# Optimization experiments

Measured on AMD Instinct MI355X. Metric: run time of the kernel, lower is better.

The kernel has to match this reference:

```python
import jax, jax.numpy as jnp
import numpy as np

B, N, D = 1, 4096, 512
H, HD = 8, 64
NBINS = 512
CAND = 64
SCALE = 1.0 / np.sqrt(HD)
MAX_NORM = 1.0 - 1e-5
TWO_PI = 2.0 * np.pi


def _project(x):
    # Poincare-ball style projection: clip L2 norm of each point to MAX_NORM.
    n = jnp.sqrt(jnp.sum(x * x, axis=-1, keepdims=True))
    s = jnp.minimum(1.0, MAX_NORM / jnp.maximum(n, 1e-12))
    return x * s


def _bins(x):
    # Deterministic geometric binning (DavisCache stand-in): quantize the
    # angle of the first two coordinates into NBINS bins.
    ang = jnp.arctan2(x[..., 1], x[..., 0])  # (-pi, pi]
    b = jnp.floor((ang / TWO_PI + 0.5) * NBINS)
    return jnp.clip(b, 0, NBINS - 1).astype(jnp.int32)


def setup_inputs() -> dict:
    key0 = jax.random.key(0)
    ks = jax.random.split(key0, 12)
    w = 0.02  # typical init scale for projection weights
    return {
        "query": jax.random.normal(ks[0], (B, N, D), dtype=jnp.float32),
        "key": jax.random.normal(ks[1], (B, N, D), dtype=jnp.float32),
        "value": jax.random.normal(ks[2], (B, N, D), dtype=jnp.float32),
        "Wq": jax.random.normal(ks[3], (D, D), dtype=jnp.float32) * w,
        "bq": jnp.zeros((D,), dtype=jnp.float32),
        "Wk": jax.random.normal(ks[4], (D, D), dtype=jnp.float32) * w,
        "bk": jnp.zeros((D,), dtype=jnp.float32),
        "Wv": jax.random.normal(ks[5], (D, D), dtype=jnp.float32) * w,
        "bv": jnp.zeros((D,), dtype=jnp.float32),
        "Wo": jax.random.normal(ks[6], (D, D), dtype=jnp.float32) * w,
        "bo": jnp.zeros((D,), dtype=jnp.float32),
    }


def reference(query, key, value, Wq, bq, Wk, bk, Wv, bv, Wo, bo):
    Bq, Nq, Dm = query.shape
    Nk = key.shape[1]
    # projections + split heads -> (B, H, N, HD)
    q = (query @ Wq.T + bq).reshape(Bq, Nq, H, HD).transpose(0, 2, 1, 3)
    k = (key @ Wk.T + bk).reshape(Bq, Nk, H, HD).transpose(0, 2, 1, 3)
    v = (value @ Wv.T + bv).reshape(Bq, Nk, H, HD).transpose(0, 2, 1, 3)
    q = _project(q)
    k = _project(k)

    # geometric binning; candidate keys for a query are those whose bin is
    # within radius 1 of the query's bin (neighboring_bins, radius=1).
    qb = _bins(q)  # (B, H, Nq) int32
    kb = _bins(k)  # (B, H, Nk) int32
    mask = jnp.abs(qb[..., :, None] - kb[..., None, :]) <= 1  # (B,H,Nq,Nk)
    # fallback: if a query has no candidates, attend over all keys
    any_valid = jnp.any(mask, axis=-1, keepdims=True)
    eff = jnp.where(any_valid, mask, True)
    # keep only the first CAND candidates per query (by key index)
    rank = jnp.cumsum(eff.astype(jnp.int32), axis=-1) - 1
    sel = eff & (rank < CAND)

    scores = jnp.einsum("bhqd,bhkd->bhqk", q, k) * SCALE
    scores = jnp.where(sel, scores, -jnp.inf)
    attn = jax.nn.softmax(scores, axis=-1)  # dropout p=0.0 (eval mode)
    out = jnp.einsum("bhqk,bhkd->bhqd", attn, v)

    out = out.transpose(0, 2, 1, 3).reshape(Bq, Nq, Dm)
    return out @ Wo.T + bo
```

## Files before the change

kernel.cpp:

```cpp
#include <hip/hip_runtime.h>
#include <math.h>

typedef unsigned short u16;
typedef __attribute__((ext_vector_type(8))) short v8bf;
typedef __attribute__((ext_vector_type(4))) float f32x4;

#define N_TOK 4096
#define DMODEL 512
#define NHEAD 8
#define HDIM 64
#define CANDN 64
#define NBINS 512
#define BINCAP 64
#define QCAP 128
#define ATT_SCALE 0.125f
#define MAX_NORM_F 0.99999f

__device__ __forceinline__ u16 f2bf(float f) {
  union { float f; unsigned int i; } v; v.f = f;
  unsigned int x = v.i;
  return (u16)((x + 0x7fffu + ((x >> 16) & 1u)) >> 16);
}
__device__ __forceinline__ uint4 pack8v(const float4 x0, const float4 x1) {
  union { u16 h[8]; uint4 u; } r;
  r.h[0] = f2bf(x0.x); r.h[1] = f2bf(x0.y); r.h[2] = f2bf(x0.z); r.h[3] = f2bf(x0.w);
  r.h[4] = f2bf(x1.x); r.h[5] = f2bf(x1.y); r.h[6] = f2bf(x1.z); r.h[7] = f2bf(x1.w);
  return r.u;
}

__device__ float fdlibm_atanf(float x) {
#pragma clang fp contract(off)
  const float atanhi[4] = {4.6364760399e-01f, 7.8539812565e-01f,
                           9.8279368877e-01f, 1.5707962513e+00f};
  const float atanlo[4] = {5.0121582440e-09f, 3.7748947079e-08f,
                           3.4473217170e-08f, 7.5497894159e-08f};
  const float aT[5] = {3.3333328366e-01f, -1.9999158382e-01f, 1.4253635705e-01f,
                       -1.0648017377e-01f, 6.1687607318e-02f};
  unsigned ix = __float_as_uint(x);
  const unsigned sign = ix >> 31;
  ix &= 0x7fffffffu;
  int id;
  float z, w, s1, s2;
  if (ix >= 0x4c800000u) {
    z = atanhi[3] + 0x1p-120f;
    return sign ? -z : z;
  }
  if (ix < 0x3ee00000u) {
    if (ix < 0x39800000u) return x;
    id = -1;
  } else {
    x = fabsf(x);
    if (ix < 0x3f980000u) {
      if (ix < 0x3f300000u) { id = 0; x = (2.0f * x - 1.0f) / (2.0f + x); }
      else                  { id = 1; x = (x - 1.0f) / (x + 1.0f); }
    } else {
      if (ix < 0x401c0000u) { id = 2; x = (x - 1.5f) / (1.0f + 1.5f * x); }
      else                  { id = 3; x = -1.0f / x; }
    }
  }
  z = x * x;
  w = z * z;
  s1 = z * (aT[0] + w * (aT[2] + w * aT[4]));
  s2 = w * (aT[1] + w * aT[3]);
  if (id < 0) return x - x * (s1 + s2);
  z = atanhi[id] - ((x * (s1 + s2) - atanlo[id]) - x);
  return sign ? -z : z;
}

__device__ float fdlibm_atan2f(float y, float x) {
#pragma clang fp contract(off)
  const float pi = 3.1415927410e+00f, pi_lo = -8.7422776573e-08f;
  const unsigned hx = __float_as_uint(x), hy = __float_as_uint(y);
  if (hx == 0x3f800000u) return fdlibm_atanf(y);
  const unsigned m = ((hy >> 31) & 1u) | ((hx >> 30) & 2u);
  const unsigned ix = hx & 0x7fffffffu, iy = hy & 0x7fffffffu;
  if (iy == 0u) {
    switch (m) { case 0: case 1: return y; case 2: return pi; default: return -pi; }
  }
  if (ix == 0u) return (m & 1u) ? -1.57079637050628662f : 1.57079637050628662f;
  float z;
  if (ix + (26u << 23) < iy) {
    z = 1.57079637050628662f;
    return (m & 1u) ? -z : z;
  }
  if ((m & 2u) && iy + (26u << 23) < ix) z = 0.0f;
  else z = fdlibm_atanf(fabsf(y / x));
  switch (m) {
    case 0: return z;
    case 1: return -z;
    case 2: return pi - (z - pi_lo);
    default: return (z - pi_lo) - pi;
  }
}

__global__ __launch_bounds__(256) void binsfix_kernel(
    const float* __restrict__ query, const float* __restrict__ key_,
    const float* __restrict__ Wq, const float* __restrict__ Wk,
    int* __restrict__ qb, int* __restrict__ kb, int* __restrict__ khist)
{
  __shared__ float xs[16 * 516];
  __shared__ float wsh[16 * 516];
  __shared__ int wle[64];
  __shared__ int wlc;
  const int blk = blockIdx.x;
  const int tid = threadIdx.x;

  if (blk >= 512) {
    int4 z4; z4.x = 0; z4.y = 0; z4.z = 0; z4.w = 0;
#pragma unroll
    for (int i = 0; i < 8; ++i) ((int4*)khist)[tid + i * 256] = z4;
    return;
  }

  const int isk  = blk >> 8;
  const int tile = blk & 255;
  const float* X = isk ? key_ : query;
  const float* W = isk ? Wk : Wq;

#pragma unroll
  for (int i = 0; i < 8; ++i) {
    const int flat = i * 1024 + tid * 4;
    const int row = flat >> 9, col = flat & 511;
    *(float4*)&xs[row * 516 + col] = *(const float4*)(X + (tile * 16 + row) * DMODEL + col);
  }
#pragma unroll
  for (int i = 0; i < 8; ++i) {
    const int f = i * 256 + tid;
    const int row = f >> 7;
    const int col = (f & 127) * 4;
    const int wrow = ((row >> 1) << 6) | (row & 1);
    *(float4*)&wsh[row * 516 + col] = *(const float4*)(W + wrow * DMODEL + col);
  }
  if (tid == 0) wlc = 0;
  __syncthreads();

  {
    const int n_local = tid >> 4;
    const int pair = tid & 15;
    const int h = pair >> 1, coord = pair & 1;
    const float* wrow = &wsh[pair * 516];
    const float* xrow = &xs[n_local * 516];

    double c0 = 0.0, c1 = 0.0, c2 = 0.0, c3 = 0.0;
#pragma unroll 4
    for (int k = 0; k < DMODEL; k += 4) {
      const float4 xv = *(const float4*)(xrow + k);
      const float4 wv = *(const float4*)(wrow + k);
      c0 = fma((double)xv.x, (double)wv.x, c0);
      c1 = fma((double)xv.y, (double)wv.y, c1);
      c2 = fma((double)xv.z, (double)wv.z, c2);
      c3 = fma((double)xv.w, (double)wv.w, c3);
    }
    const double a = (c0 + c1) + (c2 + c3);
    const double other = __shfl_xor(a, 1);
    if (coord == 0) {
      const double a0 = a, a1 = other;
      const int n = tile * 16 + n_local;
      double ang = atan2(a1, a0);
      double t = (ang / 6.283185307179586 + 0.5) * 512.0;
      int b = (int)floor(t);
      b = b < 0 ? 0 : (b > 511 ? 511 : b);

      const double r = sqrt(a0 * a0 + a1 * a1);
      const double dist = fabs(t - nearbyint(t));
      const double margin = fmin(0.45, 3.3e-4 / fmax(r, 1e-30) + 5e-5);
      if (dist < margin) {
        const int p = atomicAdd(&wlc, 1);
        if (p < 64) wle[p] = (h << 4) | n_local;
        else (isk ? kb : qb)[(h << 12) + n] = b;
      } else {
        (isk ? kb : qb)[(h << 12) + n] = b;
      }
    }
  }
  __syncthreads();

  int nw = wlc; if (nw > 64) nw = 64;
  const int w = tid >> 6, d = tid & 63;
  for (int e = w; e < nw; e += 4) {
    const int n_local2 = wle[e] & 15;
    const int h2 = wle[e] >> 4;
    const int n = tile * 16 + n_local2;
    const float* xr = &xs[n_local2 * 516];
    const float* wr = W + ((h2 << 6) + d) * DMODEL;
    float acc = 0.0f;
    for (int k = 0; k < DMODEL; k += 16) {
      const float4 xa = *(const float4*)(xr + k);
      const float4 xb = *(const float4*)(xr + k + 4);
      const float4 xc = *(const float4*)(xr + k + 8);
      const float4 xd = *(const float4*)(xr + k + 12);
      const float4 wa = *(const float4*)(wr + k);
      const float4 wb = *(const float4*)(wr + k + 4);
      const float4 wc = *(const float4*)(wr + k + 8);
      const float4 wd = *(const float4*)(wr + k + 12);
      acc = __fmaf_rn(xa.x, wa.x, acc); acc = __fmaf_rn(xa.y, wa.y, acc);
      acc = __fmaf_rn(xa.z, wa.z, acc); acc = __fmaf_rn(xa.w, wa.w, acc);
      acc = __fmaf_rn(xb.x, wb.x, acc); acc = __fmaf_rn(xb.y, wb.y, acc);
      acc = __fmaf_rn(xb.z, wb.z, acc); acc = __fmaf_rn(xb.w, wb.w, acc);
      acc = __fmaf_rn(xc.x, wc.x, acc); acc = __fmaf_rn(xc.y, wc.y, acc);
      acc = __fmaf_rn(xc.z, wc.z, acc); acc = __fmaf_rn(xc.w, wc.w, acc);
      acc = __fmaf_rn(xd.x, wd.x, acc); acc = __fmaf_rn(xd.y, wd.y, acc);
      acc = __fmaf_rn(xd.z, wd.z, acc); acc = __fmaf_rn(xd.w, wd.w, acc);
    }
    {
#pragma clang fp contract(off)
      const float sq = acc * acc;
      float rr[8];
#pragma unroll
      for (int j = 0; j < 8; ++j) rr[j] = __shfl(sq, j);
      for (int i = 8; i < 64; i += 8) {
#pragma unroll
        for (int j = 0; j < 8; ++j) rr[j] += __shfl(sq, i + j);
      }
      const float ss = ((rr[0] + rr[1]) + (rr[2] + rr[3])) +
                       ((rr[4] + rr[5]) + (rr[6] + rr[7]));
      const float nrm = __fsqrt_rn(ss);
      const float s = fminf(1.0f, 0.99999f / fmaxf(nrm, 1e-12f));
      const float c0 = __shfl(acc, 0) * s;
      const float c1 = __shfl(acc, 1) * s;
      const float cr = (float)atan2((double)c1, (double)c0);
      const float fd = fdlibm_atan2f(c1, c0);
      const float tol = fmaxf(fabsf(cr) * 6e-7f, 1e-30f);
      const float ang = (fabsf(fd - cr) <= tol) ? fd : cr;
      const float t = ((ang / 6.2831854820251465f) + 0.5f) * 512.0f;
      int b = (int)floorf(t);
      b = b < 0 ? 0 : (b > 511 ? 511 : b);
      if (d == 0) (isk ? kb : qb)[(h2 << 12) + n] = b;
    }
  }
}

__global__ __launch_bounds__(256) void gemmhist_kernel(
    const float* __restrict__ query, const float* __restrict__ key_,
    const float* __restrict__ value,
    const float* __restrict__ Wq, const float* __restrict__ Wk,
    const float* __restrict__ Wv,
    const float* __restrict__ bq, const float* __restrict__ bk,
    const float* __restrict__ bv,
    const int* __restrict__ qb, const int* __restrict__ kb,
    int* __restrict__ khist, u16* __restrict__ blist,
    int* __restrict__ qhist, u16* __restrict__ qlist,
    u16* __restrict__ Qb, u16* __restrict__ Kb, u16* __restrict__ Vb)
{
  __shared__ __align__(16) char smem[30720];
  const int blk = blockIdx.x;
  const int tid = threadIdx.x;

  if (blk >= 768) {
    const int rel = blk - 768;
    const int h = rel & 7;
    const int type = (rel >> 3) & 1;
    const int chunk = rel >> 4;
    const int* src = type ? qb : kb;
    int* hist = type ? qhist : khist;
    u16* list = type ? qlist : blist;
    const int cap = type ? QCAP : BINCAP;
    const int i = (chunk << 8) + tid;
    const int b = src[(h << 12) + i];
    const int pos = atomicAdd(&hist[(h << 9) + b], 1);
    if (pos < cap) list[((h << 9) + b) * cap + pos] = (u16)i;
    return;
  }

  u16* As = (u16*)smem;
  u16* Ws = (u16*)(smem + 10240);

  const int z = blk >> 8;
  const int rem = blk & 255;
  const int bm = (rem & 63) * 64;
  const int bn = (rem >> 6) * 128;

  const float* X  = (z == 0) ? query : (z == 1) ? key_ : value;
  const float* WF = (z == 0) ? Wq : (z == 1) ? Wk : Wv;
  const float* bias = (z == 0) ? bq : (z == 1) ? bk : bv;
  u16* O          = (z == 0) ? Qb : (z == 1) ? Kb : Vb;

  const int lane = tid & 63;
  const int wave = tid >> 6;
  const int ra  = tid >> 2;
  const int oa  = (tid & 3) * 8;
  const int wm = (wave & 1) * 32;
  const int wn = (wave >> 1) * 64;
  const int l15 = lane & 15;
  const int quad = lane >> 4;

  f32x4 acc[2][4] = {};

  float4 a0f0 = *(const float4*)(X + (bm + ra) * DMODEL + oa);
  float4 a0f1 = *(const float4*)(X + (bm + ra) * DMODEL + oa + 4);
  float4 w0f0 = *(const float4*)(WF + (bn + ra) * DMODEL + oa);
  float4 w0f1 = *(const float4*)(WF + (bn + ra) * DMODEL + oa + 4);
  float4 w1f0 = *(const float4*)(WF + (bn + ra + 64) * DMODEL + oa);
  float4 w1f1 = *(const float4*)(WF + (bn + ra + 64) * DMODEL + oa + 4);

  for (int kt = 0; kt < DMODEL; kt += 32) {
    const int p = (kt >> 5) & 1;
    *(uint4*)&As[p * 2560 + ra * 40 + oa] = pack8v(a0f0, a0f1);
    *(uint4*)&Ws[p * 5120 + ra * 40 + oa] = pack8v(w0f0, w0f1);
    *(uint4*)&Ws[p * 5120 + (ra + 64) * 40 + oa] = pack8v(w1f0, w1f1);
    __syncthreads();
    if (kt + 32 < DMODEL) {
      a0f0 = *(const float4*)(X + (bm + ra) * DMODEL + kt + 32 + oa);
      a0f1 = *(const float4*)(X + (bm + ra) * DMODEL + kt + 32 + oa + 4);
      w0f0 = *(const float4*)(WF + (bn + ra) * DMODEL + kt + 32 + oa);
      w0f1 = *(const float4*)(WF + (bn + ra) * DMODEL + kt + 32 + oa + 4);
      w1f0 = *(const float4*)(WF + (bn + ra + 64) * DMODEL + kt + 32 + oa);
      w1f1 = *(const float4*)(WF + (bn + ra + 64) * DMODEL + kt + 32 + oa + 4);
    }
    v8bf af[2], bfr[4];
#pragma unroll
    for (int i = 0; i < 2; ++i)
      af[i] = *(const v8bf*)&As[p * 2560 + (wm + i * 16 + l15) * 40 + quad * 8];
#pragma unroll
    for (int j = 0; j < 4; ++j)
      bfr[j] = *(const v8bf*)&Ws[p * 5120 + (wn + j * 16 + l15) * 40 + quad * 8];
#pragma unroll
    for (int i = 0; i < 2; ++i)
#pragma unroll
      for (int j = 0; j < 4; ++j)
        acc[i][j] = __builtin_amdgcn_mfma_f32_16x16x32_bf16(af[i], bfr[j], acc[i][j], 0, 0, 0);
  }

  float bval[4];
#pragma unroll
  for (int j = 0; j < 4; ++j) bval[j] = bias[bn + wn + j * 16 + l15];
  const int h = (bn + wn) >> 6;

#pragma unroll
  for (int i = 0; i < 2; ++i) {
#pragma unroll
    for (int r = 0; r < 4; ++r) {
      const int row = bm + wm + i * 16 + quad * 4 + r;
      float v0 = acc[i][0][r] + bval[0];
      float v1 = acc[i][1][r] + bval[1];
      float v2 = acc[i][2][r] + bval[2];
      float v3 = acc[i][3][r] + bval[3];
      if (z != 2) {
        float ss = v0 * v0 + v1 * v1 + v2 * v2 + v3 * v3;
#pragma unroll
        for (int o = 1; o < 16; o <<= 1) ss += __shfl_xor(ss, o);
        const float s = fminf(1.0f, MAX_NORM_F / fmaxf(sqrtf(ss), 1e-12f));
        v0 *= s; v1 *= s; v2 *= s; v3 *= s;
      }
      const int base = (((h << 12) + row) << 6) + l15;
      O[base +  0] = f2bf(v0); O[base + 16] = f2bf(v1);
      O[base + 32] = f2bf(v2); O[base + 48] = f2bf(v3);
    }
  }
}

__global__ __launch_bounds__(64) void attn_bin_kernel(
    const u16* __restrict__ Qb, const u16* __restrict__ Kb,
    const u16* __restrict__ Vb, const int* __restrict__ qhist,
    const u16* __restrict__ qlist, const int* __restrict__ khist,
    const u16* __restrict__ blist, u16* __restrict__ aout)
{
  __shared__ u16 kf[4 * 2 * 4 * 16 * 8];
  __shared__ u16 pf[16 * 72];
  __shared__ u16 s_cand[64];
  __shared__ int s_qg[16];

  const int hb = blockIdx.x;
  const int h = hb >> 9;
  const int b = hb & 511;
  int qcnt = qhist[hb];
  if (qcnt > QCAP) qcnt = QCAP;
  if (qcnt == 0) return;

  const int lane = threadIdx.x;
  const int l15 = lane & 15;
  const int quad = lane >> 4;

  int v0 = 0xFFFF, v1 = 0xFFFF, v2 = 0xFFFF;
  int c0 = 0, c1 = 0, c2 = 0;
  if (b > 0) {
    c0 = khist[(h << 9) + b - 1];
    if (c0 > BINCAP) c0 = BINCAP;
    if (lane < c0) v0 = (int)blist[(((h << 9) + b - 1) << 6) + lane];
  }
  {
    c1 = khist[(h << 9) + b];
    if (c1 > BINCAP) c1 = BINCAP;
    if (lane < c1) v1 = (int)blist[(((h << 9) + b) << 6) + lane];
  }
  if (b < NBINS - 1) {
    c2 = khist[(h << 9) + b + 1];
    if (c2 > BINCAP) c2 = BINCAP;
    if (lane < c2) v2 = (int)blist[(((h << 9) + b + 1) << 6) + lane];
  }

  int r0 = 0, r1 = 0, r2 = 0;
#pragma unroll 8
  for (int j = 0; j < 64; ++j) {
    const int w0 = __shfl(v0, j);
    const int w1 = __shfl(v1, j);
    const int w2 = __shfl(v2, j);
    r0 += (w0 < v0) + (w1 < v0) + (w2 < v0);
    r1 += (w0 < v1) + (w1 < v1) + (w2 < v1);
    r2 += (w0 < v2) + (w1 < v2) + (w2 < v2);
  }
  const int tot = c0 + c1 + c2;
  const int ccnt = tot < CANDN ? tot : CANDN;
  const int ccnt_eff = (tot == 0) ? 64 : ccnt;
  if (tot == 0) {
    s_cand[lane] = (u16)lane;
  } else {
    if (v0 != 0xFFFF && r0 < CANDN) s_cand[r0] = (u16)v0;
    if (v1 != 0xFFFF && r1 < CANDN) s_cand[r1] = (u16)v1;
    if (v2 != 0xFFFF && r2 < CANDN) s_cand[r2] = (u16)v2;
  }
  __syncthreads();
  if (tot > 0 && lane >= ccnt) s_cand[lane] = s_cand[0];
  __syncthreads();

  {
    const int r = lane >> 3, s = lane & 7;
    const int ks = s >> 2, qd = s & 3;
#pragma unroll
    for (int it = 0; it < 8; ++it) {
      const int key = it * 8 + r;
      const int c = s_cand[key];
      const uint4 kv = *(const uint4*)(Kb + ((h << 18) | (c << 6)) + s * 8);
      const int idx = ((((key >> 4) * 2 + ks) * 4 + qd) * 16 + (key & 15)) * 8;
      *(uint4*)&kf[idx] = kv;
    }
  }
  __syncthreads();
  v8bf akf[4][2];
#pragma unroll
  for (int t = 0; t < 4; ++t)
#pragma unroll
    for (int ks = 0; ks < 2; ++ks)
      akf[t][ks] = *(const v8bf*)&kf[(((t * 2 + ks) * 4 + quad) * 16 + l15) * 8];
  __syncthreads();

  {
    const int r = lane >> 3, s = lane & 7;
    const int nt = s >> 1, d0 = (s & 1) * 8;
#pragma unroll
    for (int it = 0; it < 8; ++it) {
      const int key = it * 8 + r;
      const int c = s_cand[key];
      union { u16 hh[8]; uint4 u; } vv;
      vv.u = *(const uint4*)(Vb + ((h << 18) | (c << 6)) + s * 8);
      const int kstep = key >> 5, qd = (key >> 3) & 3, j = key & 7;
#pragma unroll
      for (int m = 0; m < 8; ++m)
        kf[(((nt * 2 + kstep) * 4 + qd) * 16 + d0 + m) * 8 + j] = vv.hh[m];
    }
  }
  __syncthreads();
  v8bf bvf[4][2];
#pragma unroll
  for (int t = 0; t < 4; ++t)
#pragma unroll
    for (int ks = 0; ks < 2; ++ks)
      bvf[t][ks] = *(const v8bf*)&kf[(((t * 2 + ks) * 4 + quad) * 16 + l15) * 8];

  const int nchunk = (qcnt + 15) >> 4;
  for (int ci = 0; ci < nchunk; ++ci) {
    const int base = ci << 4;
    const int qcn = min(16, qcnt - base);
    __syncthreads();
    if (lane < 16) {
      int idx = base + lane;
      if (idx > qcnt - 1) idx = qcnt - 1;
      s_qg[lane] = (int)qlist[(hb << 7) + idx];
    }
    __syncthreads();

    const u16* qrow = Qb + ((h << 18) | (s_qg[l15] << 6));
    v8bf bq[2];
#pragma unroll
    for (int ks = 0; ks < 2; ++ks)
      bq[ks] = *(const v8bf*)(qrow + ks * 32 + quad * 8);

    float sc[16];
    __builtin_amdgcn_s_setprio(1);
#pragma unroll
    for (int t = 0; t < 4; ++t) {
      f32x4 sa = {0.f, 0.f, 0.f, 0.f};
      sa = __builtin_amdgcn_mfma_f32_16x16x32_bf16(akf[t][0], bq[0], sa, 0, 0, 0);
      sa = __builtin_amdgcn_mfma_f32_16x16x32_bf16(akf[t][1], bq[1], sa, 0, 0, 0);
#pragma unroll
      for (int r = 0; r < 4; ++r) {
        const int key = t * 16 + quad * 4 + r;
        sc[t * 4 + r] = (key < ccnt_eff) ? sa[r] * ATT_SCALE : -INFINITY;
      }
    }
    __builtin_amdgcn_s_setprio(0);
    float mx = sc[0];
#pragma unroll
    for (int i = 1; i < 16; ++i) mx = fmaxf(mx, sc[i]);
    mx = fmaxf(mx, __shfl_xor(mx, 16));
    mx = fmaxf(mx, __shfl_xor(mx, 32));
    float sum = 0.0f;
    float pe[16];
#pragma unroll
    for (int i = 0; i < 16; ++i) { pe[i] = __expf(sc[i] - mx); sum += pe[i]; }
    sum += __shfl_xor(sum, 16);
    sum += __shfl_xor(sum, 32);
    const float inv = 1.0f / sum;

    __syncthreads();
#pragma unroll
    for (int t = 0; t < 4; ++t)
#pragma unroll
      for (int r = 0; r < 4; ++r)
        pf[l15 * 72 + t * 16 + quad * 4 + r] = f2bf(pe[t * 4 + r] * inv);
    __syncthreads();

    v8bf ap[2];
#pragma unroll
    for (int ks = 0; ks < 2; ++ks)
      ap[ks] = *(const v8bf*)&pf[l15 * 72 + ks * 32 + quad * 8];

    __builtin_amdgcn_s_setprio(1);
#pragma unroll
    for (int nt = 0; nt < 4; ++nt) {
      f32x4 o = {0.f, 0.f, 0.f, 0.f};
      o = __builtin_amdgcn_mfma_f32_16x16x32_bf16(ap[0], bvf[nt][0], o, 0, 0, 0);
      o = __builtin_amdgcn_mfma_f32_16x16x32_bf16(ap[1], bvf[nt][1], o, 0, 0, 0);
#pragma unroll
      for (int r = 0; r < 4; ++r) {
        const int row = quad * 4 + r;
        if (row < qcn)
          aout[s_qg[row] * DMODEL + (h << 6) + nt * 16 + l15] = f2bf(o[r]);
      }
    }
    __builtin_amdgcn_s_setprio(0);
  }
}

__global__ __launch_bounds__(256) void gemm_out_kernel(
    const u16* __restrict__ A, const float* __restrict__ WF,
    const float* __restrict__ bias, float* __restrict__ O)
{
  __shared__ u16 As[2][64 * 40];
  __shared__ u16 Ws[2][64 * 40];

  const int tid  = threadIdx.x;
  const int lane = tid & 63;
  const int wave = tid >> 6;
  const int ra  = tid >> 2;
  const int oa  = (tid & 3) * 8;

  const int bm = blockIdx.x * 64;
  const int bn = blockIdx.y * 64;
  const int wm = (wave & 1) * 32;
  const int wn = (wave >> 1) * 32;
  const int l15 = lane & 15;
  const int quad = lane >> 4;

  f32x4 acc[2][2] = {};

  uint4 a0 = *(const uint4*)(A + (bm + ra) * DMODEL + oa);
  float4 w0f0 = *(const float4*)(WF + (bn + ra) * DMODEL + oa);
  float4 w0f1 = *(const float4*)(WF + (bn + ra) * DMODEL + oa + 4);

  for (int kt = 0; kt < DMODEL; kt += 32) {
    const int p = (kt >> 5) & 1;
    *(uint4*)&As[p][ra * 40 + oa] = a0;
    *(uint4*)&Ws[p][ra * 40 + oa] = pack8v(w0f0, w0f1);
    __syncthreads();
    if (kt + 32 < DMODEL) {
      a0 = *(const uint4*)(A + (bm + ra) * DMODEL + kt + 32 + oa);
      w0f0 = *(const float4*)(WF + (bn + ra) * DMODEL + kt + 32 + oa);
      w0f1 = *(const float4*)(WF + (bn + ra) * DMODEL + kt + 32 + oa + 4);
    }
    v8bf af[2], bfr[2];
#pragma unroll
    for (int i = 0; i < 2; ++i)
      af[i] = *(const v8bf*)&As[p][(wm + i * 16 + l15) * 40 + quad * 8];
#pragma unroll
    for (int j = 0; j < 2; ++j)
      bfr[j] = *(const v8bf*)&Ws[p][(wn + j * 16 + l15) * 40 + quad * 8];
#pragma unroll
    for (int i = 0; i < 2; ++i)
#pragma unroll
      for (int j = 0; j < 2; ++j)
        acc[i][j] = __builtin_amdgcn_mfma_f32_16x16x32_bf16(af[i], bfr[j], acc[i][j], 0, 0, 0);
  }

#pragma unroll
  for (int j = 0; j < 2; ++j) {
    const int cg = bn + wn + j * 16 + l15;
    const float bval = bias[cg];
#pragma unroll
    for (int i = 0; i < 2; ++i) {
      const int rbase = bm + wm + i * 16 + quad * 4;
#pragma unroll
      for (int r = 0; r < 4; ++r)
        O[(rbase + r) * DMODEL + cg] = acc[i][j][r] + bval;
    }
  }
}

extern "C" void kernel_launch(void* const* d_in, const int* in_sizes, int n_in,
                              void* d_out, int out_size, void* d_ws, size_t ws_size,
                              hipStream_t stream) {
  const float* query = (const float*)d_in[0];
  const float* key_  = (const float*)d_in[1];
  const float* value = (const float*)d_in[2];
  const float* Wq = (const float*)d_in[3];
  const float* bq = (const float*)d_in[4];
  const float* Wk = (const float*)d_in[5];
  const float* bk = (const float*)d_in[6];
  const float* Wv = (const float*)d_in[7];
  const float* bv = (const float*)d_in[8];
  const float* Wo = (const float*)d_in[9];
  const float* bo = (const float*)d_in[10];

  char* ws = (char*)d_ws;
  u16* Qb    = (u16*)(ws + 14680064);
  u16* Kb    = (u16*)(ws + 18874368);
  u16* Vb    = (u16*)(ws + 23068672);
  u16* aout  = (u16*)(ws + 27262976);
  int* qb    = (int*)(ws + 31457280);
  int* kb    = (int*)(ws + 31588352);
  int* khist = (int*)(ws + 31784960);
  int* qhist = (int*)(ws + 31801344);
  u16* blist = (u16*)(ws + 31817728);
  u16* qlist = (u16*)(ws + 32342016);

  binsfix_kernel<<<513, 256, 0, stream>>>(
      query, key_, Wq, Wk, qb, kb, khist);
  gemmhist_kernel<<<1024, 256, 0, stream>>>(
      query, key_, value, Wq, Wk, Wv, bq, bk, bv,
      qb, kb, khist, blist, qhist, qlist, Qb, Kb, Vb);
  attn_bin_kernel<<<4096, 64, 0, stream>>>(
      Qb, Kb, Vb, qhist, qlist, khist, blist, aout);
  gemm_out_kernel<<<dim3(64, 8), 256, 0, stream>>>(aout, Wo, bo, (float*)d_out);
}
```

Measured before the change: 174.4 us.

## Fuse bin computation, histogram build and QKV GEMM into one kernel launch

```diff
diff --git a/kernel.cpp b/kernel.cpp
--- a/kernel.cpp
+++ b/kernel.cpp
@@ -26,6 +26,11 @@
   r.h[0] = f2bf(x0.x); r.h[1] = f2bf(x0.y); r.h[2] = f2bf(x0.z); r.h[3] = f2bf(x0.w);
   r.h[4] = f2bf(x1.x); r.h[5] = f2bf(x1.y); r.h[6] = f2bf(x1.z); r.h[7] = f2bf(x1.w);
   return r.u;
+}
+
+__global__ __launch_bounds__(256) void zero_hist_kernel(int* __restrict__ khist) {
+  int4 z4; z4.x = 0; z4.y = 0; z4.z = 0; z4.w = 0;
+  ((int4*)khist)[(blockIdx.x << 8) + threadIdx.x] = z4;
 }
 
 __device__ float fdlibm_atanf(float x) {
@@ -93,29 +98,125 @@
   }
 }
 
-__global__ __launch_bounds__(256) void binsfix_kernel(
+__global__ __launch_bounds__(256) void fused_kernel(
     const float* __restrict__ query, const float* __restrict__ key_,
+    const float* __restrict__ value,
     const float* __restrict__ Wq, const float* __restrict__ Wk,
-    int* __restrict__ qb, int* __restrict__ kb, int* __restrict__ khist)
+    const float* __restrict__ Wv,
+    const float* __restrict__ bq, const float* __restrict__ bk,
+    const float* __restrict__ bv,
+    int* __restrict__ qb, int* __restrict__ kb,
+    int* __restrict__ khist, u16* __restrict__ blist,
+    int* __restrict__ qhist, u16* __restrict__ qlist,
+    u16* __restrict__ Qb, u16* __restrict__ Kb, u16* __restrict__ Vb)
 {
-  __shared__ float xs[16 * 516];
-  __shared__ float wsh[16 * 516];
+  __shared__ __align__(16) char smem[66304];
   __shared__ int wle[64];
   __shared__ int wlc;
   const int blk = blockIdx.x;
   const int tid = threadIdx.x;
 
   if (blk >= 512) {
-    int4 z4; z4.x = 0; z4.y = 0; z4.z = 0; z4.w = 0;
-#pragma unroll
-    for (int i = 0; i < 8; ++i) ((int4*)khist)[tid + i * 256] = z4;
+    u16* As = (u16*)smem;
+    u16* Ws = (u16*)(smem + 10240);
+
+    const int rel = blk - 512;
+    const int z = rel >> 8;
+    const int rem = rel & 255;
+    const int bm = (rem & 63) * 64;
+    const int bn = (rem >> 6) * 128;
+
+    const float* X  = (z == 0) ? query : (z == 1) ? key_ : value;
+    const float* WF = (z == 0) ? Wq : (z == 1) ? Wk : Wv;
+    const float* bias = (z == 0) ? bq : (z == 1) ? bk : bv;
+    u16* O          = (z == 0) ? Qb : (z == 1) ? Kb : Vb;
+
+    const int lane = tid & 63;
+    const int wave = tid >> 6;
+    const int ra  = tid >> 2;
+    const int oa  = (tid & 3) * 8;
+    const int wm = (wave & 1) * 32;
+    const int wn = (wave >> 1) * 64;
+    const int l15 = lane & 15;
+    const int quad = lane >> 4;
+
+    f32x4 acc[2][4] = {};
+
+    float4 a0f0 = *(const float4*)(X + (bm + ra) * DMODEL + oa);
+    float4 a0f1 = *(const float4*)(X + (bm + ra) * DMODEL + oa + 4);
+    float4 w0f0 = *(const float4*)(WF + (bn + ra) * DMODEL + oa);
+    float4 w0f1 = *(const float4*)(WF + (bn + ra) * DMODEL + oa + 4);
+    float4 w1f0 = *(const float4*)(WF + (bn + ra + 64) * DMODEL + oa);
+    float4 w1f1 = *(const float4*)(WF + (bn + ra + 64) * DMODEL + oa + 4);
+
+    for (int kt = 0; kt < DMODEL; kt += 32) {
+      const int p = (kt >> 5) & 1;
+      *(uint4*)&As[p * 2560 + ra * 40 + oa] = pack8v(a0f0, a0f1);
+      *(uint4*)&Ws[p * 5120 + ra * 40 + oa] = pack8v(w0f0, w0f1);
+      *(uint4*)&Ws[p * 5120 + (ra + 64) * 40 + oa] = pack8v(w1f0, w1f1);
+      __syncthreads();
+      if (kt + 32 < DMODEL) {
+        a0f0 = *(const float4*)(X + (bm + ra) * DMODEL + kt + 32 + oa);
+        a0f1 = *(const float4*)(X + (bm + ra) * DMODEL + kt + 32 + oa + 4);
+        w0f0 = *(const float4*)(WF + (bn + ra) * DMODEL + kt + 32 + oa);
+        w0f1 = *(const float4*)(WF + (bn + ra) * DMODEL + kt + 32 + oa + 4);
+        w1f0 = *(const float4*)(WF + (bn + ra + 64) * DMODEL + kt + 32 + oa);
+        w1f1 = *(const float4*)(WF + (bn + ra + 64) * DMODEL + kt + 32 + oa + 4);
+      }
+      v8bf af[2], bfr[4];
+#pragma unroll
+      for (int i = 0; i < 2; ++i)
+        af[i] = *(const v8bf*)&As[p * 2560 + (wm + i * 16 + l15) * 40 + quad * 8];
+#pragma unroll
+      for (int j = 0; j < 4; ++j)
+        bfr[j] = *(const v8bf*)&Ws[p * 5120 + (wn + j * 16 + l15) * 40 + quad * 8];
+#pragma unroll
+      for (int i = 0; i < 2; ++i)
+#pragma unroll
+        for (int j = 0; j < 4; ++j)
+          acc[i][j] = __builtin_amdgcn_mfma_f32_16x16x32_bf16(af[i], bfr[j], acc[i][j], 0, 0, 0);
+    }
+
+    float bval[4];
+#pragma unroll
+    for (int j = 0; j < 4; ++j) bval[j] = bias[bn + wn + j * 16 + l15];
+    const int h = (bn + wn) >> 6;
+
+#pragma unroll
+    for (int i = 0; i < 2; ++i) {
+#pragma unroll
+      for (int r = 0; r < 4; ++r) {
+        const int row = bm + wm + i * 16 + quad * 4 + r;
+        float v0 = acc[i][0][r] + bval[0];
+        float v1 = acc[i][1][r] + bval[1];
+        float v2 = acc[i][2][r] + bval[2];
+        float v3 = acc[i][3][r] + bval[3];
+        if (z != 2) {
+          float ss = v0 * v0 + v1 * v1 + v2 * v2 + v3 * v3;
+#pragma unroll
+          for (int o = 1; o < 16; o <<= 1) ss += __shfl_xor(ss, o);
+          const float s = fminf(1.0f, MAX_NORM_F / fmaxf(sqrtf(ss), 1e-12f));
+          v0 *= s; v1 *= s; v2 *= s; v3 *= s;
+        }
+        const int base = (((h << 12) + row) << 6) + l15;
+        O[base +  0] = f2bf(v0); O[base + 16] = f2bf(v1);
+        O[base + 32] = f2bf(v2); O[base + 48] = f2bf(v3);
+      }
+    }
     return;
   }
+
+  float* xs  = (float*)smem;
+  float* wsh = (float*)(smem + 33024);
 
   const int isk  = blk >> 8;
   const int tile = blk & 255;
   const float* X = isk ? key_ : query;
   const float* W = isk ? Wk : Wq;
+  int* outb  = isk ? kb : qb;
+  int* hist  = isk ? khist : qhist;
+  u16* list  = isk ? blist : qlist;
+  const int cap = isk ? BINCAP : QCAP;
 
 #pragma unroll
   for (int i = 0; i < 8; ++i) {
@@ -164,12 +265,15 @@
       const double r = sqrt(a0 * a0 + a1 * a1);
       const double dist = fabs(t - nearbyint(t));
       const double margin = fmin(0.45, 3.3e-4 / fmax(r, 1e-30) + 5e-5);
+      bool deferred = false;
       if (dist < margin) {
         const int p = atomicAdd(&wlc, 1);
-        if (p < 64) wle[p] = (h << 4) | n_local;
-        else (isk ? kb : qb)[(h << 12) + n] = b;
-      } else {
-        (isk ? kb : qb)[(h << 12) + n] = b;
+        if (p < 64) { wle[p] = (h << 4) | n_local; deferred = true; }
+      }
+      if (!deferred) {
+        outb[(h << 12) + n] = b;
+        const int pos = atomicAdd(&hist[(h << 9) + b], 1);
+        if (pos < cap) list[((h << 9) + b) * cap + pos] = (u16)n;
       }
     }
   }
@@ -225,126 +329,11 @@
       const float t = ((ang / 6.2831854820251465f) + 0.5f) * 512.0f;
       int b = (int)floorf(t);
       b = b < 0 ? 0 : (b > 511 ? 511 : b);
-      if (d == 0) (isk ? kb : qb)[(h2 << 12) + n] = b;
-    }
-  }
-}
-
-__global__ __launch_bounds__(256) void gemmhist_kernel(
-    const float* __restrict__ query, const float* __restrict__ key_,
-    const float* __restrict__ value,
-    const float* __restrict__ Wq, const float* __restrict__ Wk,
-    const float* __restrict__ Wv,
-    const float* __restrict__ bq, const float* __restrict__ bk,
-    const float* __restrict__ bv,
-    const int* __restrict__ qb, const int* __restrict__ kb,
-    int* __restrict__ khist, u16* __restrict__ blist,
-    int* __restrict__ qhist, u16* __restrict__ qlist,
-    u16* __restrict__ Qb, u16* __restrict__ Kb, u16* __restrict__ Vb)
-{
-  __shared__ __align__(16) char smem[30720];
-  const int blk = blockIdx.x;
-  const int tid = threadIdx.x;
-
-  if (blk >= 768) {
-    const int rel = blk - 768;
-    const int h = rel & 7;
-    const int type = (rel >> 3) & 1;
-    const int chunk = rel >> 4;
-    const int* src = type ? qb : kb;
-    int* hist = type ? qhist : khist;
-    u16* list = type ? qlist : blist;
-    const int cap = type ? QCAP : BINCAP;
-    const int i = (chunk << 8) + tid;
-    const int b = src[(h << 12) + i];
-    const int pos = atomicAdd(&hist[(h << 9) + b], 1);
-    if (pos < cap) list[((h << 9) + b) * cap + pos] = (u16)i;
-    return;
-  }
-
-  u16* As = (u16*)smem;
-  u16* Ws = (u16*)(smem + 10240);
-
-  const int z = blk >> 8;
-  const int rem = blk & 255;
-  const int bm = (rem & 63) * 64;
-  const int bn = (rem >> 6) * 128;
-
-  const float* X  = (z == 0) ? query : (z == 1) ? key_ : value;
-  const float* WF = (z == 0) ? Wq : (z == 1) ? Wk : Wv;
-  const float* bias = (z == 0) ? bq : (z == 1) ? bk : bv;
-  u16* O          = (z == 0) ? Qb : (z == 1) ? Kb : Vb;
-
-  const int lane = tid & 63;
-  const int wave = tid >> 6;
-  const int ra  = tid >> 2;
-  const int oa  = (tid & 3) * 8;
-  const int wm = (wave & 1) * 32;
-  const int wn = (wave >> 1) * 64;
-  const int l15 = lane & 15;
-  const int quad = lane >> 4;
-
-  f32x4 acc[2][4] = {};
-
-  float4 a0f0 = *(const float4*)(X + (bm + ra) * DMODEL + oa);
-  float4 a0f1 = *(const float4*)(X + (bm + ra) * DMODEL + oa + 4);
-  float4 w0f0 = *(const float4*)(WF + (bn + ra) * DMODEL + oa);
-  float4 w0f1 = *(const float4*)(WF + (bn + ra) * DMODEL + oa + 4);
-  float4 w1f0 = *(const float4*)(WF + (bn + ra + 64) * DMODEL + oa);
-  float4 w1f1 = *(const float4*)(WF + (bn + ra + 64) * DMODEL + oa + 4);
-
-  for (int kt = 0; kt < DMODEL; kt += 32) {
-    const int p = (kt >> 5) & 1;
-    *(uint4*)&As[p * 2560 + ra * 40 + oa] = pack8v(a0f0, a0f1);
-    *(uint4*)&Ws[p * 5120 + ra * 40 + oa] = pack8v(w0f0, w0f1);
-    *(uint4*)&Ws[p * 5120 + (ra + 64) * 40 + oa] = pack8v(w1f0, w1f1);
-    __syncthreads();
-    if (kt + 32 < DMODEL) {
-      a0f0 = *(const float4*)(X + (bm + ra) * DMODEL + kt + 32 + oa);
-      a0f1 = *(const float4*)(X + (bm + ra) * DMODEL + kt + 32 + oa + 4);
-      w0f0 = *(const float4*)(WF + (bn + ra) * DMODEL + kt + 32 + oa);
-      w0f1 = *(const float4*)(WF + (bn + ra) * DMODEL + kt + 32 + oa + 4);
-      w1f0 = *(const float4*)(WF + (bn + ra + 64) * DMODEL + kt + 32 + oa);
-      w1f1 = *(const float4*)(WF + (bn + ra + 64) * DMODEL + kt + 32 + oa + 4);
-    }
-    v8bf af[2], bfr[4];
-#pragma unroll
-    for (int i = 0; i < 2; ++i)
-      af[i] = *(const v8bf*)&As[p * 2560 + (wm + i * 16 + l15) * 40 + quad * 8];
-#pragma unroll
-    for (int j = 0; j < 4; ++j)
-      bfr[j] = *(const v8bf*)&Ws[p * 5120 + (wn + j * 16 + l15) * 40 + quad * 8];
-#pragma unroll
-    for (int i = 0; i < 2; ++i)
-#pragma unroll
-      for (int j = 0; j < 4; ++j)
-        acc[i][j] = __builtin_amdgcn_mfma_f32_16x16x32_bf16(af[i], bfr[j], acc[i][j], 0, 0, 0);
-  }
-
-  float bval[4];
-#pragma unroll
-  for (int j = 0; j < 4; ++j) bval[j] = bias[bn + wn + j * 16 + l15];
-  const int h = (bn + wn) >> 6;
-
-#pragma unroll
-  for (int i = 0; i < 2; ++i) {
-#pragma unroll
-    for (int r = 0; r < 4; ++r) {
-      const int row = bm + wm + i * 16 + quad * 4 + r;
-      float v0 = acc[i][0][r] + bval[0];
-      float v1 = acc[i][1][r] + bval[1];
-      float v2 = acc[i][2][r] + bval[2];
-      float v3 = acc[i][3][r] + bval[3];
-      if (z != 2) {
-        float ss = v0 * v0 + v1 * v1 + v2 * v2 + v3 * v3;
-#pragma unroll
-        for (int o = 1; o < 16; o <<= 1) ss += __shfl_xor(ss, o);
-        const float s = fminf(1.0f, MAX_NORM_F / fmaxf(sqrtf(ss), 1e-12f));
-        v0 *= s; v1 *= s; v2 *= s; v3 *= s;
-      }
-      const int base = (((h << 12) + row) << 6) + l15;
-      O[base +  0] = f2bf(v0); O[base + 16] = f2bf(v1);
-      O[base + 32] = f2bf(v2); O[base + 48] = f2bf(v3);
+      if (d == 0) {
+        outb[(h2 << 12) + n] = b;
+        const int pos = atomicAdd(&hist[(h2 << 9) + b], 1);
+        if (pos < cap) list[((h2 << 9) + b) * cap + pos] = (u16)n;
+      }
     }
   }
 }
@@ -623,9 +612,8 @@
   u16* blist = (u16*)(ws + 31817728);
   u16* qlist = (u16*)(ws + 32342016);
 
-  binsfix_kernel<<<513, 256, 0, stream>>>(
-      query, key_, Wq, Wk, qb, kb, khist);
-  gemmhist_kernel<<<1024, 256, 0, stream>>>(
+  zero_hist_kernel<<<8, 256, 0, stream>>>(khist);
+  fused_kernel<<<1280, 256, 0, stream>>>(
       query, key_, value, Wq, Wk, Wv, bq, bk, bv,
       qb, kb, khist, blist, qhist, qlist, Qb, Kb, Vb);
   attn_bin_kernel<<<4096, 64, 0, stream>>>(
```

New measurement: 170.7 us. -2.1%, faster.
